# Optimization experiments

Hardware: AMD Instinct MI355X
Metric: run time of the kernel (lower is better)

The kernel has to match this reference:

```python
import jax, jax.numpy as jnp
import numpy as np

B, T, C = 2, 2048, 1024
H = 16
D = C // H  # head_dim = 64
ROPE_BASE = 10000.0


def _rope_tables(seq_len, dim, dtype=jnp.float32):
    inv_freq = 1.0 / (ROPE_BASE ** (jnp.arange(0, dim, 2, dtype=jnp.float32) / dim))
    t = jnp.arange(seq_len, dtype=jnp.float32)
    freqs = jnp.einsum('i,j->ij', t, inv_freq)          # [T, D/2]
    emb = jnp.concatenate([freqs, freqs], axis=-1)      # [T, D]
    return jnp.cos(emb).astype(dtype), jnp.sin(emb).astype(dtype)


def _rotate_half(x):
    x1, x2 = jnp.split(x, 2, axis=-1)
    return jnp.concatenate([-x2, x1], axis=-1)


def setup_inputs() -> dict:
    key = jax.random.key(0)
    ks = jax.random.split(key, 9)
    s = 0.02
    return {
        'x': jax.random.normal(ks[0], (B, T, C), jnp.float32),
        'Wq': jax.random.normal(ks[1], (C, C), jnp.float32) * s,
        'bq': jax.random.normal(ks[2], (C,), jnp.float32) * s,
        'Wk': jax.random.normal(ks[3], (C, C), jnp.float32) * s,
        'bk': jax.random.normal(ks[4], (C,), jnp.float32) * s,
        'Wv': jax.random.normal(ks[5], (C, C), jnp.float32) * s,
        'bv': jax.random.normal(ks[6], (C,), jnp.float32) * s,
        'Wo': jax.random.normal(ks[7], (C, C), jnp.float32) * s,
        'bo': jax.random.normal(ks[8], (C,), jnp.float32) * s,
    }


def reference(x, Wq, bq, Wk, bk, Wv, bv, Wo, bo):
    b, t, c = x.shape
    q = x @ Wq.T + bq
    k = x @ Wk.T + bk
    v = x @ Wv.T + bv
    # [B, H, T, D]
    q = q.reshape(b, t, H, D).transpose(0, 2, 1, 3)
    k = k.reshape(b, t, H, D).transpose(0, 2, 1, 3)
    v = v.reshape(b, t, H, D).transpose(0, 2, 1, 3)
    cos, sin = _rope_tables(t, D, x.dtype)  # [T, D]
    q = q * cos + _rotate_half(q) * sin
    k = k * cos + _rotate_half(k) * sin
    scale = 1.0 / jnp.sqrt(jnp.array(D, x.dtype))
    scores = jnp.einsum('bhqd,bhkd->bhqk', q, k) * scale
    causal = jnp.triu(jnp.full((t, t), -jnp.inf, dtype=x.dtype), k=1)
    scores = scores + causal
    attn = jax.nn.softmax(scores, axis=-1)
    out = jnp.einsum('bhqk,bhkd->bhqd', attn, v)
    out = out.transpose(0, 2, 1, 3).reshape(b, t, c)
    return out @ Wo.T + bo
```

## Files before the change

### kernel.cpp

```cpp
#include <hip/hip_runtime.h>


typedef unsigned short u16;
typedef unsigned int u32;
typedef __bf16 bf16_t;
typedef bf16_t bf16x8 __attribute__((ext_vector_type(8)));
typedef float f32x4 __attribute__((ext_vector_type(4)));
typedef float f32x16 __attribute__((ext_vector_type(16)));

#if __has_builtin(__builtin_amdgcn_exp2f)
#define EXP2(x) __builtin_amdgcn_exp2f(x)
#else
#define EXP2(x) exp2f(x)
#endif

__device__ __forceinline__ u16 f2bf(float f) {
  union { float f; unsigned u; } v; v.f = f;
  return (u16)((v.u + 0x7FFFu + ((v.u >> 16) & 1u)) >> 16);
}

__device__ __forceinline__ void gload_lds16(const void* g, void* l) {
  __builtin_amdgcn_global_load_lds(
      (const __attribute__((address_space(1))) void*)g,
      (__attribute__((address_space(3))) void*)l, 16, 0, 0);
}

__global__ __launch_bounds__(256) void prep_kernel(
    const float* __restrict__ x, const float* __restrict__ Wq,
    const float* __restrict__ Wk, const float* __restrict__ Wv,
    const float* __restrict__ Wo, const float* __restrict__ bq,
    const float* __restrict__ bk, const float* __restrict__ bv,
    u16* __restrict__ xb, u16* __restrict__ Wqkvo, float* __restrict__ tab,
    float* __restrict__ bcat) {
  const int bid = blockIdx.x, tid = threadIdx.x;
  if (bid < 4096) {
    int i = bid * 256 + tid;
    float4 f = ((const float4*)x)[i];
    ushort4 o;
    o.x = f2bf(f.x); o.y = f2bf(f.y); o.z = f2bf(f.z); o.w = f2bf(f.w);
    ((ushort4*)xb)[i] = o;
  } else if (bid < 8192) {
    int wsel = (bid - 4096) >> 10;
    int i = ((bid - 4096) & 1023) * 256 + tid;
    const float* in = (wsel == 0) ? Wq : (wsel == 1) ? Wk : (wsel == 2) ? Wv : Wo;
    float4 f = ((const float4*)in)[i];
    ushort4 o;
    o.x = f2bf(f.x); o.y = f2bf(f.y); o.z = f2bf(f.z); o.w = f2bf(f.w);
    ((ushort4*)(Wqkvo + (size_t)wsel * 1048576))[i] = o;
  } else if (bid < 8448) {
    int idx = (bid - 8192) * 256 + tid;
    int t = idx >> 5, i = idx & 31;
    float freq = powf(10000.0f, -(float)i * (1.0f / 32.0f));
    float a = (float)t * freq;
    tab[t * 64 + i] = cosf(a);
    tab[t * 64 + 32 + i] = sinf(a);
  } else {
    int j = (bid - 8448) * 256 + tid;
    float v = (j < 1024) ? bq[j] : (j < 2048) ? bk[j - 1024] : bv[j - 2048];
    bcat[j] = v;
  }
}

__device__ __forceinline__ void stage256(const u16* __restrict__ A,
                                         const u16* __restrict__ Bt,
                                         int m0, int n0, int k0,
                                         u16* lA, u16* lB, int tid) {
#pragma unroll
  for (int r = 0; r < 4; ++r) {
    int ch = r * 512 + tid;
    int row = ch >> 3, s = ch & 7;
    gload_lds16(A + (size_t)(m0 + row) * 1024 + k0 + ((s ^ (row & 7)) << 3),
                lA + ch * 8);
  }
#pragma unroll
  for (int r = 0; r < 4; ++r) {
    int ch = r * 512 + tid;
    int row = ch >> 3, s = ch & 7;
    gload_lds16(Bt + (size_t)(n0 + row) * 1024 + k0 + ((s ^ (row & 7)) << 3),
                lB + ch * 8);
  }
}

__device__ __forceinline__ void gemm256_db(const u16* __restrict__ A,
                                           const u16* __restrict__ Bt,
                                           int m0, int n0, u16* lA, u16* lB,
                                           f32x4 acc[8][4]) {
  const int tid = threadIdx.x;
  const int l = tid & 63;
  const int wid = tid >> 6, wr = wid >> 2, wc = wid & 3;

#pragma unroll
  for (int m = 0; m < 8; ++m)
#pragma unroll
    for (int n = 0; n < 4; ++n)
      acc[m][n] = (f32x4){0.f, 0.f, 0.f, 0.f};

  stage256(A, Bt, m0, n0, 0, lA, lB, tid);

  int cur = 0;
  for (int t = 0; t < 16; ++t) {
    if (t + 1 < 16) {
      stage256(A, Bt, m0, n0, (t + 1) * 64, lA + (cur ^ 1) * 16384,
               lB + (cur ^ 1) * 16384, tid);
      asm volatile("s_waitcnt vmcnt(8)" ::: "memory");
    } else {
      asm volatile("s_waitcnt vmcnt(0)" ::: "memory");
    }
    __builtin_amdgcn_s_barrier();

    const u16* pA = lA + cur * 16384;
    const u16* pB = lB + cur * 16384;
#pragma unroll
    for (int kk = 0; kk < 2; ++kk) {
      bf16x8 af[8], bf[4];
#pragma unroll
      for (int m = 0; m < 8; ++m) {
        int row = wr * 128 + m * 16 + (l & 15);
        int slot = (kk * 4 + (l >> 4)) ^ (row & 7);
        af[m] = *(const bf16x8*)(pA + row * 64 + slot * 8);
      }
#pragma unroll
      for (int n = 0; n < 4; ++n) {
        int row = wc * 64 + n * 16 + (l & 15);
        int slot = (kk * 4 + (l >> 4)) ^ (row & 7);
        bf[n] = *(const bf16x8*)(pB + row * 64 + slot * 8);
      }
#pragma unroll
      for (int m = 0; m < 8; ++m)
#pragma unroll
        for (int n = 0; n < 4; ++n)
          acc[m][n] =
              __builtin_amdgcn_mfma_f32_16x16x32_bf16(af[m], bf[n], acc[m][n], 0, 0, 0);
    }
    __builtin_amdgcn_s_barrier();
    cur ^= 1;
  }
}

__global__ __launch_bounds__(512, 2) void qkv_kernel(
    const u16* __restrict__ xb, const u16* __restrict__ Wqkv,
    const float* __restrict__ bcat, const float* __restrict__ tab,
    u16* __restrict__ Q, u16* __restrict__ Kr, u16* __restrict__ Vt) {
  __shared__ __align__(16) u16 lds[65536];
  const int bid = blockIdx.x;
  const int tile = (bid & 7) * 24 + (bid >> 3);
  const int m0 = (tile / 12) * 256, n0 = (tile % 12) * 256;

  f32x4 acc[8][4];
  gemm256_db(xb, Wqkv, m0, n0, lds, lds + 32768, acc);

  const int tid = threadIdx.x, l = tid & 63;
  const int wid = tid >> 6, wr = wid >> 2, wc = wid & 3;
  const int gcb = n0 + wc * 64;
  const int z = gcb >> 10, h = (gcb >> 6) & 15;
  const int grb = m0 + wr * 128;
  const int b2 = grb >> 11, t0 = grb & 2047;
  u16* myl = lds + wid * 8192;

  if (z < 2) {
#pragma unroll
    for (int m = 0; m < 8; ++m)
#pragma unroll
      for (int n = 0; n < 4; ++n)
#pragma unroll
        for (int jr = 0; jr < 4; ++jr) {
          int tl = m * 16 + ((l >> 4) << 2) + jr;
          int d = n * 16 + (l & 15);
          int t = t0 + tl;
          float val = acc[m][n][jr] + bcat[gcb + d];
          float p = acc[m][n ^ 2][jr] + bcat[gcb + (d ^ 32)];
          float cs = tab[t * 64 + (d & 31)];
          float sn = tab[t * 64 + 32 + (d & 31)];
          float rot = (d < 32) ? -p : p;
          float o = val * cs + rot * sn;
          if (z == 0) o *= 0.18033688011112042f;
          myl[tl * 64 + d] = f2bf(o);
        }
    asm volatile("s_waitcnt lgkmcnt(0)" ::: "memory");
    u16* dstb = ((z == 0) ? Q : Kr) + (((size_t)(b2 * 16 + h) << 11) + t0) * 64;
#pragma unroll
    for (int i = 0; i < 16; ++i) {
      int c = i * 64 + l;
      *(bf16x8*)(dstb + c * 8) = *(const bf16x8*)(myl + c * 8);
    }
  } else {
#pragma unroll
    for (int m = 0; m < 8; ++m)
#pragma unroll
      for (int n = 0; n < 4; ++n)
#pragma unroll
        for (int jr = 0; jr < 4; ++jr) {
          int tl = m * 16 + ((l >> 4) << 2) + jr;
          int d = n * 16 + (l & 15);
          float val = acc[m][n][jr] + bcat[gcb + d];
          myl[d * 128 + (tl ^ ((d & 7) << 4))] = f2bf(val);
        }
    asm volatile("s_waitcnt lgkmcnt(0)" ::: "memory");
#pragma unroll
    for (int i = 0; i < 16; ++i) {
      int c = i * 64 + l;
      int d = c >> 4, off = (c & 15) * 8;
      bf16x8 v = *(const bf16x8*)(myl + d * 128 + (off ^ ((d & 7) << 4)));
      *(bf16x8*)(Vt + (((size_t)((b2 * 16 + h) * 64 + d)) << 11) + t0 + off) = v;
    }
  }
}

__global__ __launch_bounds__(512, 2) void outproj_kernel(
    const u16* __restrict__ attn, const u16* __restrict__ Wob,
    const float* __restrict__ bo, float* __restrict__ out) {
  __shared__ __align__(16) u16 lds[65536];
  const int bid = blockIdx.x;
  const int tile = (bid & 7) * 8 + (bid >> 3);
  const int m0 = (tile / 4) * 256, n0 = (tile % 4) * 256;
  f32x4 acc[8][4];
  gemm256_db(attn, Wob, m0, n0, lds, lds + 32768, acc);
  const int tid = threadIdx.x, l = tid & 63;
  const int wid = tid >> 6, wr = wid >> 2, wc = wid & 3;
#pragma unroll
  for (int m = 0; m < 8; ++m)
#pragma unroll
    for (int n = 0; n < 4; ++n)
#pragma unroll
      for (int jr = 0; jr < 4; ++jr) {
        int gr = m0 + wr * 128 + m * 16 + ((l >> 4) << 2) + jr;
        int gc = n0 + wc * 64 + n * 16 + (l & 15);
        out[(size_t)gr * 1024 + gc] = acc[m][n][jr] + bo[gc];
      }
}

__global__ __launch_bounds__(512) void attn_kernel(const u16* __restrict__ Q,
                                                   const u16* __restrict__ K,
                                                   const u16* __restrict__ Vt,
                                                   u16* __restrict__ out) {
  __shared__ __align__(16) u16 lK[2][2][4096];
  __shared__ __align__(16) u16 lV[2][2][4096];
  const int tid = threadIdx.x, l = tid & 63;
  const int w8 = tid >> 6;
  const int grp = w8 >> 2, w = w8 & 3;
  const int gtid = tid & 255;
  const int n = blockIdx.x;
  const int xcd = n & 7, j = n >> 3;
  const int bh = xcd * 4 + (j & 3);
  const int ji = j >> 2;
  const int qb = (ji < 8) ? (15 - ji) : (ji - 8);
  const int b = bh >> 4, h = bh & 15;
  const int lq = l & 31, hl = l >> 5;
  const int q0w = qb * 128 + w * 32;
  const int qg = q0w + lq;

  const u16* qbase = Q + ((((size_t)bh) << 11) + qg) * 64 + hl * 8;
  bf16x8 qf[4];
#pragma unroll
  for (int kd = 0; kd < 4; ++kd) qf[kd] = *(const bf16x8*)(qbase + kd * 16);

  const f32x16 z16 = {0.f, 0.f, 0.f, 0.f, 0.f, 0.f, 0.f, 0.f,
                      0.f, 0.f, 0.f, 0.f, 0.f, 0.f, 0.f, 0.f};
  f32x16 oacc[2];
  oacc[0] = z16; oacc[1] = z16;
  float mi = -1e30f, li = 0.f;

  const int nth = qb + 1;
  const int tb = grp * nth;

#define STAGE_KV(it_, buf_)                                                        \
  {                                                                                \
    _Pragma("unroll") for (int r = 0; r < 2; ++r) {                                \
      int ch = r * 256 + gtid;                                                     \
      int row = ch >> 3, s = ch & 7;                                               \
      gload_lds16(                                                                 \
          K + ((((size_t)bh) << 11) + (it_) * 64 + row) * 64 + ((s ^ (row & 7)) << 3), \
          &lK[grp][buf_][0] + ch * 8);                                             \
    }                                                                              \
    _Pragma("unroll") for (int r = 0; r < 2; ++r) {                                \
      int ch = r * 256 + gtid;                                                     \
      int row = ch >> 3, s = ch & 7;                                               \
      gload_lds16(                                                                 \
          Vt + ((((size_t)bh) * 64 + row) << 11) + (it_) * 64 + ((s ^ (row & 7)) << 3), \
          &lV[grp][buf_][0] + ch * 8);                                             \
    }                                                                              \
  }

  STAGE_KV(tb, 0);
  int cur = 0;

  for (int it = 0; it < nth; ++it) {
    const int tile = tb + it;
    const int kv0 = tile * 64;
    if (it + 1 < nth) {
      STAGE_KV(tile + 1, cur ^ 1);
      asm volatile("s_waitcnt vmcnt(4)" ::: "memory");
    } else {
      asm volatile("s_waitcnt vmcnt(0)" ::: "memory");
    }
    __builtin_amdgcn_s_barrier();

    const bool active = (kv0 <= q0w + 31);
    if (active) {
      const u16* pK = &lK[grp][cur][0];
      const u16* pV = &lV[grp][cur][0];

      f32x16 sacc[2];
      sacc[0] = z16; sacc[1] = z16;
#pragma unroll
      for (int g = 0; g < 2; ++g) {
        int row = g * 32 + lq;
        int sw = row & 7;
#pragma unroll
        for (int kd = 0; kd < 4; ++kd) {
          bf16x8 kf = *(const bf16x8*)(pK + row * 64 + (((kd * 2 + hl) ^ sw) << 3));
          sacc[g] = __builtin_amdgcn_mfma_f32_32x32x16_bf16(kf, qf[kd], sacc[g], 0, 0, 0);
        }
      }

      if (kv0 + 63 > q0w) {
#pragma unroll
        for (int g = 0; g < 2; ++g)
#pragma unroll
          for (int r = 0; r < 16; ++r) {
            int kv = kv0 + g * 32 + (r & 3) + ((r >> 2) << 3) + hl * 4;
            if (kv > qg) sacc[g][r] = -1e30f;
          }
      }

      float mx[16];
#pragma unroll
      for (int r = 0; r < 16; ++r) mx[r] = fmaxf(sacc[0][r], sacc[1][r]);
#pragma unroll
      for (int s = 8; s > 0; s >>= 1)
#pragma unroll
        for (int r = 0; r < s; ++r) mx[r] = fmaxf(mx[r], mx[r + s]);
      float mt = fmaxf(mx[0], __shfl_xor(mx[0], 32, 64));

      if (!__all(mt <= mi + 8.0f)) {
        float mn = fmaxf(mi, mt);
        float al = EXP2(mi - mn);
        mi = mn;
#pragma unroll
        for (int dblk = 0; dblk < 2; ++dblk)
#pragma unroll
          for (int r = 0; r < 16; ++r) oacc[dblk][r] *= al;
        li *= al;
      }
#pragma unroll
      for (int g = 0; g < 2; ++g)
#pragma unroll
        for (int r = 0; r < 16; ++r) sacc[g][r] = EXP2(sacc[g][r] - mi);
      float sm[16];
#pragma unroll
      for (int r = 0; r < 16; ++r) sm[r] = sacc[0][r] + sacc[1][r];
#pragma unroll
      for (int s = 8; s > 0; s >>= 1)
#pragma unroll
        for (int r = 0; r < s; ++r) sm[r] += sm[r + s];
      float rs = sm[0] + __shfl_xor(sm[0], 32, 64);
      li += rs;

      u32 pw[2][8], px[2][8];
#pragma unroll
      for (int g = 0; g < 2; ++g)
#pragma unroll
        for (int i = 0; i < 8; ++i) {
          union { bf16_t h2[2]; u32 u; } pk;
          pk.h2[0] = (bf16_t)sacc[g][2 * i];
          pk.h2[1] = (bf16_t)sacc[g][2 * i + 1];
          pw[g][i] = pk.u;
        }
#pragma unroll
      for (int g = 0; g < 2; ++g)
#pragma unroll
        for (int i = 0; i < 8; ++i)
          px[g][i] = (u32)__shfl_xor((int)pw[g][i], 32, 64);

      bf16x8 pfrag[4];
#pragma unroll
      for (int km = 0; km < 4; ++km) {
        const int g = km >> 1, o = (km & 1) * 4;
        union { u32 u[4]; bf16x8 v; } f;
        f.u[0] = hl ? px[g][o + 2] : pw[g][o + 0];
        f.u[1] = hl ? px[g][o + 3] : pw[g][o + 1];
        f.u[2] = hl ? pw[g][o + 2] : px[g][o + 0];
        f.u[3] = hl ? pw[g][o + 3] : px[g][o + 1];
        pfrag[km] = f.v;
      }

#pragma unroll
      for (int dblk = 0; dblk < 2; ++dblk) {
        int row = dblk * 32 + lq;
        int sw = row & 7;
#pragma unroll
        for (int km = 0; km < 4; ++km) {
          bf16x8 vf = *(const bf16x8*)(pV + row * 64 + (((km * 2 + hl) ^ sw) << 3));
          oacc[dblk] = __builtin_amdgcn_mfma_f32_32x32x16_bf16(vf, pfrag[km],
                                                              oacc[dblk], 0, 0, 0);
        }
      }
    }
    __builtin_amdgcn_s_barrier();
    cur ^= 1;
  }
#undef STAGE_KV

  float* cb = (float*)&lK[0][0][0];
  float* ml = (float*)&lV[0][0][0];
  if (grp == 1) {
    float* myo = cb + w * 2048;
#pragma unroll
    for (int dblk = 0; dblk < 2; ++dblk)
#pragma unroll
      for (int r = 0; r < 16; ++r) {
        int d = dblk * 32 + (r & 3) + ((r >> 2) << 3) + hl * 4;
        myo[d * 32 + lq] = oacc[dblk][r];
      }
    ml[w * 64 + lq] = mi;
    ml[w * 64 + 32 + lq] = li;
  }
  asm volatile("s_waitcnt lgkmcnt(0)" ::: "memory");
  __builtin_amdgcn_s_barrier();

  if (grp == 0) {
    const float m1 = ml[w * 64 + lq];
    const float l1 = ml[w * 64 + 32 + lq];
    const float* po = cb + w * 2048;
    const float m = fmaxf(mi, m1);
    const float w0 = EXP2(mi - m), w1 = EXP2(m1 - m);
    const float inv = 1.0f / (li * w0 + l1 * w1);
    const size_t rowbase = ((size_t)(b * 2048 + qg)) * 1024 + h * 64;
#pragma unroll
    for (int dblk = 0; dblk < 2; ++dblk)
#pragma unroll
      for (int g4 = 0; g4 < 4; ++g4) {
        ushort4 st;
#pragma unroll
        for (int jj = 0; jj < 4; ++jj) {
          int r = g4 * 4 + jj;
          int d = dblk * 32 + g4 * 8 + hl * 4 + jj;
          float o = (oacc[dblk][r] * w0 + po[d * 32 + lq] * w1) * inv;
          ((u16*)&st)[jj] = f2bf(o);
        }
        *(ushort4*)((u16*)out + rowbase + dblk * 32 + g4 * 8 + hl * 4) = st;
      }
  }
}

extern "C" void kernel_launch(void* const* d_in, const int* in_sizes, int n_in,
                              void* d_out, int out_size, void* d_ws, size_t ws_size,
                              hipStream_t stream) {
  const float* x  = (const float*)d_in[0];
  const float* Wq = (const float*)d_in[1];
  const float* bq = (const float*)d_in[2];
  const float* Wk = (const float*)d_in[3];
  const float* bk = (const float*)d_in[4];
  const float* Wv = (const float*)d_in[5];
  const float* bv = (const float*)d_in[6];
  const float* Wo = (const float*)d_in[7];
  const float* bo = (const float*)d_in[8];
  float* out = (float*)d_out;

  char* ws = (char*)d_ws;
  u16* xb    = (u16*)(ws);
  u16* Wqkvo = (u16*)(ws + (8ull << 20));
  u16* Wob   = Wqkvo + 3 * 1048576;
  u16* Qr  = (u16*)(ws + (16ull << 20));
  u16* Kr  = (u16*)(ws + (24ull << 20));
  u16* Vt  = (u16*)(ws + (32ull << 20));
  u16* At  = (u16*)(ws + (40ull << 20));
  float* tab  = (float*)(ws + (48ull << 20));
  float* bcat = (float*)(ws + (48ull << 20) + (512ull << 10));

  prep_kernel<<<dim3(8460), dim3(256), 0, stream>>>(x, Wq, Wk, Wv, Wo, bq, bk, bv,
                                                    xb, Wqkvo, tab, bcat);
  qkv_kernel<<<dim3(192), dim3(512), 0, stream>>>(xb, Wqkvo, bcat, tab,
                                                  Qr, Kr, Vt);
  attn_kernel<<<dim3(512), dim3(512), 0, stream>>>(Qr, Kr, Vt, At);
  outproj_kernel<<<dim3(64), dim3(512), 0, stream>>>(At, Wob, bo, out);
}
```

Baseline: 128.5 us.

## Halve attention block size to 64 query rows, drop KV double buffering, add setprio

The attention kernel now uses 256-thread blocks covering 64 query rows each, launched as 1024 blocks instead of 512. The KV range is split evenly between two wave groups, with a new interleaved block-to-q-tile ordering to balance causal work. The LDS double buffer is removed, which halves shared memory per block so more blocks fit per CU, but each tile load is now waited on synchronously. s_setprio is raised around the MFMA sections to favour matrix issue. Each KV tile is loaded once per 64 query rows instead of once per 128, so total K/V traffic goes up.

```diff
diff --git a/kernel.cpp b/kernel.cpp
--- a/kernel.cpp
+++ b/kernel.cpp
@@ -229,24 +229,25 @@
       }
 }
 
-__global__ __launch_bounds__(512) void attn_kernel(const u16* __restrict__ Q,
+__global__ __launch_bounds__(256) void attn_kernel(const u16* __restrict__ Q,
                                                    const u16* __restrict__ K,
                                                    const u16* __restrict__ Vt,
                                                    u16* __restrict__ out) {
-  __shared__ __align__(16) u16 lK[2][2][4096];
-  __shared__ __align__(16) u16 lV[2][2][4096];
+  __shared__ __align__(16) u16 lK[2][4096];
+  __shared__ __align__(16) u16 lV[2][4096];
   const int tid = threadIdx.x, l = tid & 63;
-  const int w8 = tid >> 6;
-  const int grp = w8 >> 2, w = w8 & 3;
-  const int gtid = tid & 255;
+  const int w4 = tid >> 6;
+  const int grp = w4 >> 1, wq = w4 & 1;
+  const int gtid = tid & 127;
   const int n = blockIdx.x;
-  const int xcd = n & 7, j = n >> 3;
-  const int bh = xcd * 4 + (j & 3);
-  const int ji = j >> 2;
-  const int qb = (ji < 8) ? (15 - ji) : (ji - 8);
+  const int bh = (n & 7) * 4 + ((n >> 3) & 3);
+  const int r5 = n >> 5;
+  const int rr = r5 & 7, k4 = r5 >> 3;
+  const int qj = (k4 == 0) ? (31 - rr) : (k4 == 1) ? (23 - rr)
+               : (k4 == 2) ? rr : (8 + rr);
   const int b = bh >> 4, h = bh & 15;
   const int lq = l & 31, hl = l >> 5;
-  const int q0w = qb * 128 + w * 32;
+  const int q0w = qj * 64 + wq * 32;
   const int qg = q0w + lq;
 
   const u16* qbase = Q + ((((size_t)bh) << 11) + qg) * 64 + hl * 8;
@@ -260,48 +261,43 @@
   oacc[0] = z16; oacc[1] = z16;
   float mi = -1e30f, li = 0.f;
 
-  const int nth = qb + 1;
-  const int tb = grp * nth;
-
-#define STAGE_KV(it_, buf_)                                                        \
+  const int nt = qj + 1;
+  const int nh = (nt + 1) >> 1;
+  const int tb = grp * nh;
+
+#define STAGE_KV(it_)                                                              \
   {                                                                                \
-    _Pragma("unroll") for (int r = 0; r < 2; ++r) {                                \
-      int ch = r * 256 + gtid;                                                     \
+    _Pragma("unroll") for (int r = 0; r < 4; ++r) {                                \
+      int ch = r * 128 + gtid;                                                     \
       int row = ch >> 3, s = ch & 7;                                               \
       gload_lds16(                                                                 \
           K + ((((size_t)bh) << 11) + (it_) * 64 + row) * 64 + ((s ^ (row & 7)) << 3), \
-          &lK[grp][buf_][0] + ch * 8);                                             \
+          &lK[grp][0] + ch * 8);                                                   \
     }                                                                              \
-    _Pragma("unroll") for (int r = 0; r < 2; ++r) {                                \
-      int ch = r * 256 + gtid;                                                     \
+    _Pragma("unroll") for (int r = 0; r < 4; ++r) {                                \
+      int ch = r * 128 + gtid;                                                     \
       int row = ch >> 3, s = ch & 7;                                               \
       gload_lds16(                                                                 \
           Vt + ((((size_t)bh) * 64 + row) << 11) + (it_) * 64 + ((s ^ (row & 7)) << 3), \
-          &lV[grp][buf_][0] + ch * 8);                                             \
+          &lV[grp][0] + ch * 8);                                                   \
     }                                                                              \
   }
 
-  STAGE_KV(tb, 0);
-  int cur = 0;
-
-  for (int it = 0; it < nth; ++it) {
+  for (int it = 0; it < nh; ++it) {
     const int tile = tb + it;
     const int kv0 = tile * 64;
-    if (it + 1 < nth) {
-      STAGE_KV(tile + 1, cur ^ 1);
-      asm volatile("s_waitcnt vmcnt(4)" ::: "memory");
-    } else {
-      asm volatile("s_waitcnt vmcnt(0)" ::: "memory");
-    }
+    STAGE_KV(tile);
+    asm volatile("s_waitcnt vmcnt(0)" ::: "memory");
     __builtin_amdgcn_s_barrier();
 
     const bool active = (kv0 <= q0w + 31);
     if (active) {
-      const u16* pK = &lK[grp][cur][0];
-      const u16* pV = &lV[grp][cur][0];
+      const u16* pK = &lK[grp][0];
+      const u16* pV = &lV[grp][0];
 
       f32x16 sacc[2];
       sacc[0] = z16; sacc[1] = z16;
+      __builtin_amdgcn_s_setprio(1);
 #pragma unroll
       for (int g = 0; g < 2; ++g) {
         int row = g * 32 + lq;
@@ -312,6 +308,7 @@
           sacc[g] = __builtin_amdgcn_mfma_f32_32x32x16_bf16(kf, qf[kd], sacc[g], 0, 0, 0);
         }
       }
+      __builtin_amdgcn_s_setprio(0);
 
       if (kv0 + 63 > q0w) {
 #pragma unroll
@@ -384,6 +381,7 @@
         pfrag[km] = f.v;
       }
 
+      __builtin_amdgcn_s_setprio(1);
 #pragma unroll
       for (int dblk = 0; dblk < 2; ++dblk) {
         int row = dblk * 32 + lq;
@@ -395,16 +393,16 @@
                                                               oacc[dblk], 0, 0, 0);
         }
       }
+      __builtin_amdgcn_s_setprio(0);
     }
     __builtin_amdgcn_s_barrier();
-    cur ^= 1;
   }
 #undef STAGE_KV
 
-  float* cb = (float*)&lK[0][0][0];
-  float* ml = (float*)&lV[0][0][0];
+  float* cb = (float*)&lK[0][0];
+  float* ml = (float*)&lV[0][0];
   if (grp == 1) {
-    float* myo = cb + w * 2048;
+    float* myo = cb + wq * 2048;
 #pragma unroll
     for (int dblk = 0; dblk < 2; ++dblk)
 #pragma unroll
@@ -412,16 +410,16 @@
         int d = dblk * 32 + (r & 3) + ((r >> 2) << 3) + hl * 4;
         myo[d * 32 + lq] = oacc[dblk][r];
       }
-    ml[w * 64 + lq] = mi;
-    ml[w * 64 + 32 + lq] = li;
+    ml[wq * 64 + lq] = mi;
+    ml[wq * 64 + 32 + lq] = li;
   }
   asm volatile("s_waitcnt lgkmcnt(0)" ::: "memory");
   __builtin_amdgcn_s_barrier();
 
   if (grp == 0) {
-    const float m1 = ml[w * 64 + lq];
-    const float l1 = ml[w * 64 + 32 + lq];
-    const float* po = cb + w * 2048;
+    const float m1 = ml[wq * 64 + lq];
+    const float l1 = ml[wq * 64 + 32 + lq];
+    const float* po = cb + wq * 2048;
     const float m = fmaxf(mi, m1);
     const float w0 = EXP2(mi - m), w1 = EXP2(m1 - m);
     const float inv = 1.0f / (li * w0 + l1 * w1);
@@ -472,6 +470,6 @@
                                                     xb, Wqkvo, tab, bcat);
   qkv_kernel<<<dim3(192), dim3(512), 0, stream>>>(xb, Wqkvo, bcat, tab,
                                                   Qr, Kr, Vt);
-  attn_kernel<<<dim3(512), dim3(512), 0, stream>>>(Qr, Kr, Vt, At);
+  attn_kernel<<<dim3(1024), dim3(256), 0, stream>>>(Qr, Kr, Vt, At);
   outproj_kernel<<<dim3(64), dim3(512), 0, stream>>>(At, Wob, bo, out);
 }
```

After: 132.1 us. 1.03x slower.
